# Performance work log

Hardware: AMD Instinct MI355X
Metric: run time of the kernel (lower is better)

## Reference

```python
import jax, jax.numpy as jnp
import numpy as np

N = 100000   # nodes
E = 1000000  # edges
DIN = 64
DH = 128     # num_hidden == out_dim
EPS = 1e-5


def setup_inputs() -> dict:
    key = jax.random.key(0)
    ks = jax.random.split(key, 16)
    x = jax.random.normal(ks[0], (N, DIN), jnp.float32)
    src = jax.random.randint(ks[1], (E,), 0, N)
    dst = jax.random.randint(ks[2], (E,), 0, N)
    dims = [(DIN, DH), (DH, DH), (DH, DH)]
    inp = {"x": x, "src": src, "dst": dst}
    for l, (di, do) in enumerate(dims):
        s = 1.0 / np.sqrt(di)
        inp[f"w_self{l}"] = jax.random.normal(ks[3 + 4 * l], (di, do), jnp.float32) * s
        inp[f"w_neigh{l}"] = jax.random.normal(ks[4 + 4 * l], (di, do), jnp.float32) * s
        inp[f"b{l}"] = jnp.zeros((do,), jnp.float32)
    # layernorm affine params for layers 0 and 1 (last layer has norm=None)
    for l in (0, 1):
        inp[f"g{l}"] = jnp.ones((DH,), jnp.float32)
        inp[f"be{l}"] = jnp.zeros((DH,), jnp.float32)
    return inp


def _layernorm(h, g, b):
    mu = jnp.mean(h, axis=-1, keepdims=True)
    var = jnp.mean(jnp.square(h - mu), axis=-1, keepdims=True)
    return (h - mu) * jax.lax.rsqrt(var + EPS) * g + b


def _sage_layer(h, src, dst, w_self, w_neigh, b, gamma, beta):
    # mean aggregation over incoming edges (DGL copy_u + mean)
    msg = h[src]                                            # [E, d_in]
    agg = jax.ops.segment_sum(msg, dst, num_segments=N)     # [N, d_in]
    deg = jax.ops.segment_sum(jnp.ones((E,), h.dtype), dst, num_segments=N)
    h_neigh = agg / jnp.where(deg > 0, deg, 1.0)[:, None]
    out = h @ w_self + h_neigh @ w_neigh + b
    out = jax.nn.relu(out)  # DGL applies activation before norm
    if gamma is not None:
        out = _layernorm(out, gamma, beta)
    return out


def reference(x, src, dst,
              w_self0, w_neigh0, b0,
              w_self1, w_neigh1, b1,
              w_self2, w_neigh2, b2,
              g0, be0, g1, be1):
    h = x  # dropout is identity in eval mode
    h = _sage_layer(h, src, dst, w_self0, w_neigh0, b0, g0, be0)
    h = _sage_layer(h, src, dst, w_self1, w_neigh1, b1, g1, be1)
    h = _sage_layer(h, src, dst, w_self2, w_neigh2, b2, None, None)
    return h
```

## Files before the change

kernel.cpp:

```cpp
#include <hip/hip_runtime.h>

#define NN   100000
#define NE   1000000
#define EPS  1e-5f
#define CAP  32
#define CPAD 16

typedef unsigned short ushort_t;
typedef unsigned int   uint_t;
typedef __attribute__((ext_vector_type(8))) __bf16 bf16x8;
typedef __attribute__((ext_vector_type(4))) float  f32x4;

static __device__ __forceinline__ ushort_t f2bf(float f) {
    uint_t u = __float_as_uint(f);
    u = u + 0x7fff + ((u >> 16) & 1);
    return (ushort_t)(u >> 16);
}
static __device__ __forceinline__ float bf2f(uint_t us) {
    return __uint_as_float(us << 16);
}

#define HALF_E 500000
#define EBH    1954
#define XBN    12500
#define WB0    64
#define WB1    128
#define PREP_BLOCKS (EBH + XBN + WB0 + WB1 + WB1)

static __device__ __forceinline__ void wprep_body(const float* __restrict__ wsf,
                                                  const float* __restrict__ wng,
                                                  __bf16* __restrict__ Bt, int DIN, int idx) {
    int K = 2 * DIN;
    if (idx >= 128 * K) return;
    int col = idx / K;
    int k   = idx % K;
    float v = (k < DIN) ? wsf[k * 128 + col] : wng[(k - DIN) * 128 + col];
    Bt[idx] = (__bf16)v;
}

__global__ __launch_bounds__(256) void k_prep(const int* __restrict__ src,
                                              const int* __restrict__ dst,
                                              int* __restrict__ cnt,
                                              int* __restrict__ slots,
                                              const float* __restrict__ x,
                                              ushort_t* __restrict__ xb,
                                              const float* __restrict__ ws0, const float* __restrict__ wn0, __bf16* __restrict__ Bt0,
                                              const float* __restrict__ ws1, const float* __restrict__ wn1, __bf16* __restrict__ Bt1,
                                              const float* __restrict__ ws2, const float* __restrict__ wn2, __bf16* __restrict__ Bt2) {
    int b = blockIdx.x;
    if (b < EBH) {
        int i = b * 256 + threadIdx.x;
        if (i < HALF_E) {
            int d0 = dst[i];
            int d1 = dst[i + HALF_E];
            int s0 = src[i];
            int s1 = src[i + HALF_E];
            int p0 = atomicAdd(&cnt[d0 * CPAD], 1);
            int p1 = atomicAdd(&cnt[d1 * CPAD], 1);
            if (p0 < CAP) __builtin_nontemporal_store(s0, &slots[d0 * CAP + p0]);
            if (p1 < CAP) __builtin_nontemporal_store(s1, &slots[d1 * CAP + p1]);
        }
        return;
    }
    b -= EBH;
    if (b < XBN) {
        int i = b * 256 + threadIdx.x;
        if (i < NN * 32) {
            float2 v = *(const float2*)(x + (size_t)i * 2);
            uint_t pk = (uint_t)f2bf(v.x) | ((uint_t)f2bf(v.y) << 16);
            *(uint_t*)(xb + (size_t)i * 2) = pk;
        }
        return;
    }
    b -= XBN;
    if (b < WB0) { wprep_body(ws0, wn0, Bt0, 64,  b * 256 + threadIdx.x); return; }
    b -= WB0;
    if (b < WB1) { wprep_body(ws1, wn1, Bt1, 128, b * 256 + threadIdx.x); return; }
    b -= WB1;
    wprep_body(ws2, wn2, Bt2, 128, b * 256 + threadIdx.x);
}

template <int DIN, bool DO_LN, bool OUT_F32>
__global__ __launch_bounds__(512, 4) void k_fused(const ushort_t* __restrict__ ha,
                                                  const int* __restrict__ slots,
                                                  const int* __restrict__ cnt,
                                                  const __bf16* __restrict__ Bt,
                                                  const float* __restrict__ bias,
                                                  const float* __restrict__ gamma,
                                                  const float* __restrict__ beta,
                                                  void* __restrict__ out) {
    constexpr int K     = 2 * DIN;
    constexpr int KS2   = DIN / 32;
    constexpr int EL    = (DIN == 64) ? 4 : 8;
    constexpr int PITCH = DIN + 8;
    int lane = threadIdx.x & 63;
    int w    = threadIdx.x >> 6;
    int n16  = lane & 15;
    int q    = lane >> 4;
    int base = blockIdx.x * 64;

    __shared__ float C[64 * 132];
    ushort_t* agg = (ushort_t*)C;

    int nb0  = w * 8;
    int degv = 0;
    if (lane < 8) {
        int nd = base + nb0 + lane;
        degv = (nd < NN) ? cnt[nd * CPAD] : 0;
    }
#pragma unroll
    for (int p = 0; p < 4; ++p) {
        int la = nb0 + 2 * p, lb = la + 1;
        int na = base + la,   nb = base + lb;
        int dega = __shfl(degv, 2 * p);
        int degb = __shfl(degv, 2 * p + 1);
        int ca = dega < CAP ? dega : CAP;
        int cb = degb < CAP ? degb : CAP;
        const int* sla = slots + (size_t)(na < NN ? na : NN - 1) * CAP;
        const int* slb = slots + (size_t)(nb < NN ? nb : NN - 1) * CAP;
        const int* slp = (lane < 32) ? sla : slb;
        int ivab = slp[lane & 31];

        float aa[EL], ab[EL];
#pragma unroll
        for (int k = 0; k < EL; ++k) { aa[k] = 0.f; ab[k] = 0.f; }

        int cam1 = ca > 0 ? ca - 1 : 0;
        int cbm1 = cb > 0 ? cb - 1 : 0;
        int cmax = ca > cb ? ca : cb;
        for (int t = 0; t < cmax; t += 8) {
#pragma unroll
            for (int hh = 0; hh < 2; ++hh) {
                int r  = t + hh * 4 + q;
                int ia = r < ca ? r : cam1;
                int ib = r < cb ? r : cbm1;
                int sa = __shfl(ivab, ia);
                int sb = __shfl(ivab, 32 + ib);
                if (r < ca) {
                    if (DIN == 64) {
                        uint2 v = *(const uint2*)(ha + (size_t)sa * 64 + n16 * 4);
                        aa[0] += bf2f(v.x & 0xffffu); aa[1] += bf2f(v.x >> 16);
                        aa[2] += bf2f(v.y & 0xffffu); aa[3] += bf2f(v.y >> 16);
                    } else {
                        uint4 v = *(const uint4*)(ha + (size_t)sa * 128 + n16 * 8);
                        aa[0] += bf2f(v.x & 0xffffu); aa[1] += bf2f(v.x >> 16);
                        aa[2] += bf2f(v.y & 0xffffu); aa[3] += bf2f(v.y >> 16);
                        aa[4] += bf2f(v.z & 0xffffu); aa[5] += bf2f(v.z >> 16);
                        aa[6] += bf2f(v.w & 0xffffu); aa[7] += bf2f(v.w >> 16);
                    }
                }
                if (r < cb) {
                    if (DIN == 64) {
                        uint2 v = *(const uint2*)(ha + (size_t)sb * 64 + n16 * 4);
                        ab[0] += bf2f(v.x & 0xffffu); ab[1] += bf2f(v.x >> 16);
                        ab[2] += bf2f(v.y & 0xffffu); ab[3] += bf2f(v.y >> 16);
                    } else {
                        uint4 v = *(const uint4*)(ha + (size_t)sb * 128 + n16 * 8);
                        ab[0] += bf2f(v.x & 0xffffu); ab[1] += bf2f(v.x >> 16);
                        ab[2] += bf2f(v.y & 0xffffu); ab[3] += bf2f(v.y >> 16);
                        ab[4] += bf2f(v.z & 0xffffu); ab[5] += bf2f(v.z >> 16);
                        ab[6] += bf2f(v.w & 0xffffu); ab[7] += bf2f(v.w >> 16);
                    }
                }
            }
        }
#pragma unroll
        for (int k = 0; k < EL; ++k) {
            aa[k] += __shfl_xor(aa[k], 16); aa[k] += __shfl_xor(aa[k], 32);
            ab[k] += __shfl_xor(ab[k], 16); ab[k] += __shfl_xor(ab[k], 32);
        }
        if (lane < 16) {
            float inva = 1.0f / (float)(dega > 0 ? dega : 1);
            float invb = 1.0f / (float)(degb > 0 ? degb : 1);
            if (DIN == 64) {
                uint2 oa, ob;
                oa.x = (uint_t)f2bf(aa[0] * inva) | ((uint_t)f2bf(aa[1] * inva) << 16);
                oa.y = (uint_t)f2bf(aa[2] * inva) | ((uint_t)f2bf(aa[3] * inva) << 16);
                ob.x = (uint_t)f2bf(ab[0] * invb) | ((uint_t)f2bf(ab[1] * invb) << 16);
                ob.y = (uint_t)f2bf(ab[2] * invb) | ((uint_t)f2bf(ab[3] * invb) << 16);
                *(uint2*)(agg + (size_t)la * PITCH + lane * 4) = oa;
                *(uint2*)(agg + (size_t)lb * PITCH + lane * 4) = ob;
            } else {
                uint4 oa, ob;
                oa.x = (uint_t)f2bf(aa[0] * inva) | ((uint_t)f2bf(aa[1] * inva) << 16);
                oa.y = (uint_t)f2bf(aa[2] * inva) | ((uint_t)f2bf(aa[3] * inva) << 16);
                oa.z = (uint_t)f2bf(aa[4] * inva) | ((uint_t)f2bf(aa[5] * inva) << 16);
                oa.w = (uint_t)f2bf(aa[6] * inva) | ((uint_t)f2bf(aa[7] * inva) << 16);
                ob.x = (uint_t)f2bf(ab[0] * invb) | ((uint_t)f2bf(ab[1] * invb) << 16);
                ob.y = (uint_t)f2bf(ab[2] * invb) | ((uint_t)f2bf(ab[3] * invb) << 16);
                ob.z = (uint_t)f2bf(ab[4] * invb) | ((uint_t)f2bf(ab[5] * invb) << 16);
                ob.w = (uint_t)f2bf(ab[6] * invb) | ((uint_t)f2bf(ab[7] * invb) << 16);
                *(uint4*)(agg + (size_t)la * PITCH + lane * 8) = oa;
                *(uint4*)(agg + (size_t)lb * PITCH + lane * 8) = ob;
            }
        }
    }
    __syncthreads();

    bf16x8 Bs[2][KS2];
#pragma unroll
    for (int hh = 0; hh < 2; ++hh)
#pragma unroll
        for (int ks = 0; ks < KS2; ++ks) {
            int col = w * 16 + n16;
            int k   = hh * DIN + ks * 32 + q * 8;
            Bs[hh][ks] = *(const bf16x8*)(Bt + (size_t)col * K + k);
        }

    int rowc[4];
#pragma unroll
    for (int ng = 0; ng < 4; ++ng) {
        int row  = base + ng * 16 + n16;
        rowc[ng] = row < NN ? row : NN - 1;
    }

    f32x4 acc[4] = {};

#pragma unroll
    for (int ks = 0; ks < KS2; ++ks) {
        bf16x8 a[4];
#pragma unroll
        for (int ng = 0; ng < 4; ++ng)
            a[ng] = *(const bf16x8*)(ha + (size_t)rowc[ng] * DIN + ks * 32 + q * 8);
#pragma unroll
        for (int ng = 0; ng < 4; ++ng)
            acc[ng] = __builtin_amdgcn_mfma_f32_16x16x32_bf16(a[ng], Bs[0][ks], acc[ng], 0, 0, 0);
    }
#pragma unroll
    for (int ks = 0; ks < KS2; ++ks) {
        bf16x8 a[4];
#pragma unroll
        for (int ng = 0; ng < 4; ++ng)
            a[ng] = *(const bf16x8*)(agg + (size_t)(ng * 16 + n16) * PITCH + ks * 32 + q * 8);
#pragma unroll
        for (int ng = 0; ng < 4; ++ng)
            acc[ng] = __builtin_amdgcn_mfma_f32_16x16x32_bf16(a[ng], Bs[1][ks], acc[ng], 0, 0, 0);
    }
    __syncthreads();

    {
        float bv = bias[w * 16 + n16];
#pragma unroll
        for (int ng = 0; ng < 4; ++ng)
#pragma unroll
            for (int r = 0; r < 4; ++r) {
                float v = acc[ng][r] + bv;
                C[(ng * 16 + q * 4 + r) * 132 + w * 16 + n16] = fmaxf(v, 0.f);
            }
    }
    __syncthreads();

    float g0v = 0.f, g1v = 0.f, b0v = 0.f, b1v = 0.f;
    if (DO_LN) {
        g0v = gamma[lane]; g1v = gamma[64 + lane];
        b0v = beta[lane];  b1v = beta[64 + lane];
    }
    for (int rr = 0; rr < 8; ++rr) {
        int lrow = w * 8 + rr;
        int node = base + lrow;
        if (node >= NN) break;
        float a0 = C[lrow * 132 + lane];
        float a1 = C[lrow * 132 + 64 + lane];
        float o0 = a0, o1 = a1;
        if (DO_LN) {
            float s = a0 + a1, qq = a0 * a0 + a1 * a1;
#pragma unroll
            for (int m = 1; m < 64; m <<= 1) {
                s  += __shfl_xor(s, m);
                qq += __shfl_xor(qq, m);
            }
            float mu  = s * (1.f / 128.f);
            float var = qq * (1.f / 128.f) - mu * mu;
            float rs  = rsqrtf(var + EPS);
            o0 = (a0 - mu) * rs * g0v + b0v;
            o1 = (a1 - mu) * rs * g1v + b1v;
        }
        if (OUT_F32) {
            ((float*)out)[(size_t)node * 128 + lane]      = o0;
            ((float*)out)[(size_t)node * 128 + 64 + lane] = o1;
        } else {
            ((ushort_t*)out)[(size_t)node * 128 + lane]      = f2bf(o0);
            ((ushort_t*)out)[(size_t)node * 128 + 64 + lane] = f2bf(o1);
        }
    }
}

extern "C" void kernel_launch(void* const* d_in, const int* in_sizes, int n_in,
                              void* d_out, int out_size, void* d_ws, size_t ws_size,
                              hipStream_t stream) {
    const float* x   = (const float*)d_in[0];
    const int*   src = (const int*)d_in[1];
    const int*   dst = (const int*)d_in[2];
    const float* ws0 = (const float*)d_in[3];
    const float* wn0 = (const float*)d_in[4];
    const float* b0  = (const float*)d_in[5];
    const float* ws1 = (const float*)d_in[6];
    const float* wn1 = (const float*)d_in[7];
    const float* b1  = (const float*)d_in[8];
    const float* ws2 = (const float*)d_in[9];
    const float* wn2 = (const float*)d_in[10];
    const float* b2  = (const float*)d_in[11];
    const float* g0  = (const float*)d_in[12];
    const float* be0 = (const float*)d_in[13];
    const float* g1  = (const float*)d_in[14];
    const float* be1 = (const float*)d_in[15];
    (void)in_sizes; (void)n_in; (void)out_size; (void)ws_size;

    char*  ws  = (char*)d_ws;
    size_t off = 0;
    auto alloc = [&](size_t bytes) -> void* {
        void* p = ws + off;
        off = (off + bytes + 255) & ~(size_t)255;
        return p;
    };
    ushort_t* xb     = (ushort_t*)alloc((size_t)NN * 64 * 2);
    ushort_t* h1b    = (ushort_t*)alloc((size_t)NN * 128 * 2);
    ushort_t* h2b    = (ushort_t*)alloc((size_t)NN * 128 * 2);
    int*      slots  = (int*)alloc((size_t)NN * CAP * 4);
    int*      cnt    = (int*)alloc((size_t)NN * CPAD * 4);
    __bf16*   Bt0    = (__bf16*)alloc(128 * 128 * 2);
    __bf16*   Bt1    = (__bf16*)alloc(128 * 256 * 2);
    __bf16*   Bt2    = (__bf16*)alloc(128 * 256 * 2);

    const int GB = (NN + 63) / 64;

    hipMemsetAsync(cnt, 0, (size_t)NN * CPAD * 4, stream);
    k_prep<<<PREP_BLOCKS, 256, 0, stream>>>(src, dst, cnt, slots, x, xb,
                                            ws0, wn0, Bt0, ws1, wn1, Bt1, ws2, wn2, Bt2);

    k_fused<64, true, false><<<GB, 512, 0, stream>>>(xb, slots, cnt, Bt0, b0, g0, be0, h1b);
    k_fused<128, true, false><<<GB, 512, 0, stream>>>(h1b, slots, cnt, Bt1, b1, g1, be1, h2b);
    k_fused<128, false, true><<<GB, 512, 0, stream>>>(h2b, slots, cnt, Bt2, b2, nullptr, nullptr, d_out);
}
```

Baseline: 435.8 us.

## Compact degree counters, interleave edge-scatter blocks with conversion blocks, guard slot loads

Removes the 16-int padding on the per-node degree counters, so the memset shrinks and counter reads in the fused kernel become dense. The prep grid is reordered so every eighth block does edge scatter while the other seven do x conversion and weight transposition, which spreads atomic traffic across the launch instead of front-loading it. Slot loads in the fused kernel are now skipped for lanes beyond the node's degree, avoiding reads of uninitialised slots. Dense counters risk more atomic contention on shared cache lines, and PREP_P must cover all edge and conversion blocks.

```diff
diff --git a/kernel.cpp b/kernel.cpp
--- a/kernel.cpp
+++ b/kernel.cpp
@@ -4,7 +4,6 @@
 #define NE   1000000
 #define EPS  1e-5f
 #define CAP  32
-#define CPAD 16
 
 typedef unsigned short ushort_t;
 typedef unsigned int   uint_t;
@@ -25,7 +24,7 @@
 #define XBN    12500
 #define WB0    64
 #define WB1    128
-#define PREP_BLOCKS (EBH + XBN + WB0 + WB1 + WB1)
+#define PREP_P 16384
 
 static __device__ __forceinline__ void wprep_body(const float* __restrict__ wsf,
                                                   const float* __restrict__ wng,
@@ -48,23 +47,25 @@
                                               const float* __restrict__ ws1, const float* __restrict__ wn1, __bf16* __restrict__ Bt1,
                                               const float* __restrict__ ws2, const float* __restrict__ wn2, __bf16* __restrict__ Bt2) {
     int b = blockIdx.x;
-    if (b < EBH) {
-        int i = b * 256 + threadIdx.x;
+    if ((b & 7) == 0) {
+        int fb = b >> 3;
+        if (fb >= EBH) return;
+        int i = fb * 256 + threadIdx.x;
         if (i < HALF_E) {
             int d0 = dst[i];
             int d1 = dst[i + HALF_E];
             int s0 = src[i];
             int s1 = src[i + HALF_E];
-            int p0 = atomicAdd(&cnt[d0 * CPAD], 1);
-            int p1 = atomicAdd(&cnt[d1 * CPAD], 1);
+            int p0 = atomicAdd(&cnt[d0], 1);
+            int p1 = atomicAdd(&cnt[d1], 1);
             if (p0 < CAP) __builtin_nontemporal_store(s0, &slots[d0 * CAP + p0]);
             if (p1 < CAP) __builtin_nontemporal_store(s1, &slots[d1 * CAP + p1]);
         }
         return;
     }
-    b -= EBH;
-    if (b < XBN) {
-        int i = b * 256 + threadIdx.x;
+    int ob = (b >> 3) * 7 + (b & 7) - 1;
+    if (ob < XBN) {
+        int i = ob * 256 + threadIdx.x;
         if (i < NN * 32) {
             float2 v = *(const float2*)(x + (size_t)i * 2);
             uint_t pk = (uint_t)f2bf(v.x) | ((uint_t)f2bf(v.y) << 16);
@@ -72,12 +73,12 @@
         }
         return;
     }
-    b -= XBN;
-    if (b < WB0) { wprep_body(ws0, wn0, Bt0, 64,  b * 256 + threadIdx.x); return; }
-    b -= WB0;
-    if (b < WB1) { wprep_body(ws1, wn1, Bt1, 128, b * 256 + threadIdx.x); return; }
-    b -= WB1;
-    wprep_body(ws2, wn2, Bt2, 128, b * 256 + threadIdx.x);
+    ob -= XBN;
+    if (ob < WB0) { wprep_body(ws0, wn0, Bt0, 64,  ob * 256 + threadIdx.x); return; }
+    ob -= WB0;
+    if (ob < WB1) { wprep_body(ws1, wn1, Bt1, 128, ob * 256 + threadIdx.x); return; }
+    ob -= WB1;
+    if (ob < WB1) { wprep_body(ws2, wn2, Bt2, 128, ob * 256 + threadIdx.x); }
 }
 
 template <int DIN, bool DO_LN, bool OUT_F32>
@@ -106,7 +107,7 @@
     int degv = 0;
     if (lane < 8) {
         int nd = base + nb0 + lane;
-        degv = (nd < NN) ? cnt[nd * CPAD] : 0;
+        degv = (nd < NN) ? cnt[nd] : 0;
     }
 #pragma unroll
     for (int p = 0; p < 4; ++p) {
@@ -119,7 +120,9 @@
         const int* sla = slots + (size_t)(na < NN ? na : NN - 1) * CAP;
         const int* slb = slots + (size_t)(nb < NN ? nb : NN - 1) * CAP;
         const int* slp = (lane < 32) ? sla : slb;
-        int ivab = slp[lane & 31];
+        int lim = (lane < 32) ? ca : cb;
+        int ivab = 0;
+        if ((lane & 31) < lim) ivab = slp[lane & 31];
 
         float aa[EL], ab[EL];
 #pragma unroll
@@ -317,16 +320,16 @@
     ushort_t* h1b    = (ushort_t*)alloc((size_t)NN * 128 * 2);
     ushort_t* h2b    = (ushort_t*)alloc((size_t)NN * 128 * 2);
     int*      slots  = (int*)alloc((size_t)NN * CAP * 4);
-    int*      cnt    = (int*)alloc((size_t)NN * CPAD * 4);
+    int*      cnt    = (int*)alloc((size_t)NN * 4);
     __bf16*   Bt0    = (__bf16*)alloc(128 * 128 * 2);
     __bf16*   Bt1    = (__bf16*)alloc(128 * 256 * 2);
     __bf16*   Bt2    = (__bf16*)alloc(128 * 256 * 2);
 
     const int GB = (NN + 63) / 64;
 
-    hipMemsetAsync(cnt, 0, (size_t)NN * CPAD * 4, stream);
-    k_prep<<<PREP_BLOCKS, 256, 0, stream>>>(src, dst, cnt, slots, x, xb,
-                                            ws0, wn0, Bt0, ws1, wn1, Bt1, ws2, wn2, Bt2);
+    hipMemsetAsync(cnt, 0, (size_t)NN * 4, stream);
+    k_prep<<<PREP_P, 256, 0, stream>>>(src, dst, cnt, slots, x, xb,
+                                       ws0, wn0, Bt0, ws1, wn1, Bt1, ws2, wn2, Bt2);
 
     k_fused<64, true, false><<<GB, 512, 0, stream>>>(xb, slots, cnt, Bt0, b0, g0, be0, h1b);
     k_fused<128, true, false><<<GB, 512, 0, stream>>>(h1b, slots, cnt, Bt1, b1, g1, be1, h2b);
```

New measurement: 462.1 us. 1.06x slower.

## Pre-bin edges by destination range before building adjacency slots

Applied to the files above, without the earlier changes.

Adds a binning kernel that partitions edges into 8 destination buckets of 12500 nodes, packing local dst and src into one word, using shared-memory counters and one global atomic per bucket per block. The slot-fill pass then reads each bucket in chunks, so the atomics on the count array and the scattered slot writes land in a localized node range that can stay cache-resident. The count array is no longer padded per node. This adds an extra kernel launch and an extra pass over the edges, and edges beyond a bucket's fixed capacity would be dropped.

```diff
diff --git a/kernel.cpp b/kernel.cpp
--- a/kernel.cpp
+++ b/kernel.cpp
@@ -4,7 +4,6 @@
 #define NE   1000000
 #define EPS  1e-5f
 #define CAP  32
-#define CPAD 16
 
 typedef unsigned short ushort_t;
 typedef unsigned int   uint_t;
@@ -22,10 +21,47 @@
 
 #define HALF_E 500000
 #define EBH    1954
+#define BCAP   131072
+#define BUCKN  12500
+
+__global__ __launch_bounds__(256) void k_bin(const int* __restrict__ src,
+                                             const int* __restrict__ dst,
+                                             int* __restrict__ cur,
+                                             uint_t* __restrict__ binned) {
+    __shared__ int bc[8];
+    __shared__ int bb[8];
+    int t = threadIdx.x;
+    if (t < 8) bc[t] = 0;
+    __syncthreads();
+    int i = blockIdx.x * 256 + t;
+    int g0 = 0, g1 = 0, l0 = 0, l1 = 0;
+    uint_t p0 = 0, p1 = 0;
+    bool ok = (i < HALF_E);
+    if (ok) {
+        int d0 = dst[i], d1 = dst[i + HALF_E];
+        int s0 = src[i], s1 = src[i + HALF_E];
+        g0 = d0 / BUCKN;  g1 = d1 / BUCKN;
+        p0 = ((uint_t)(d0 - g0 * BUCKN) << 17) | (uint_t)s0;
+        p1 = ((uint_t)(d1 - g1 * BUCKN) << 17) | (uint_t)s1;
+        l0 = atomicAdd(&bc[g0], 1);
+        l1 = atomicAdd(&bc[g1], 1);
+    }
+    __syncthreads();
+    if (t < 8) bb[t] = atomicAdd(&cur[t], bc[t]);
+    __syncthreads();
+    if (ok) {
+        int x0 = bb[g0] + l0;
+        int x1 = bb[g1] + l1;
+        if (x0 < BCAP) binned[(size_t)g0 * BCAP + x0] = p0;
+        if (x1 < BCAP) binned[(size_t)g1 * BCAP + x1] = p1;
+    }
+}
+
+#define FBL    2048
 #define XBN    12500
 #define WB0    64
 #define WB1    128
-#define PREP_BLOCKS (EBH + XBN + WB0 + WB1 + WB1)
+#define PREP_BLOCKS (FBL + XBN + WB0 + WB1 + WB1)
 
 static __device__ __forceinline__ void wprep_body(const float* __restrict__ wsf,
                                                   const float* __restrict__ wng,
@@ -38,8 +74,8 @@
     Bt[idx] = (__bf16)v;
 }
 
-__global__ __launch_bounds__(256) void k_prep(const int* __restrict__ src,
-                                              const int* __restrict__ dst,
+__global__ __launch_bounds__(256) void k_prep(const uint_t* __restrict__ binned,
+                                              const int* __restrict__ cur,
                                               int* __restrict__ cnt,
                                               int* __restrict__ slots,
                                               const float* __restrict__ x,
@@ -48,21 +84,25 @@
                                               const float* __restrict__ ws1, const float* __restrict__ wn1, __bf16* __restrict__ Bt1,
                                               const float* __restrict__ ws2, const float* __restrict__ wn2, __bf16* __restrict__ Bt2) {
     int b = blockIdx.x;
-    if (b < EBH) {
-        int i = b * 256 + threadIdx.x;
-        if (i < HALF_E) {
-            int d0 = dst[i];
-            int d1 = dst[i + HALF_E];
-            int s0 = src[i];
-            int s1 = src[i + HALF_E];
-            int p0 = atomicAdd(&cnt[d0 * CPAD], 1);
-            int p1 = atomicAdd(&cnt[d1 * CPAD], 1);
-            if (p0 < CAP) __builtin_nontemporal_store(s0, &slots[d0 * CAP + p0]);
-            if (p1 < CAP) __builtin_nontemporal_store(s1, &slots[d1 * CAP + p1]);
+    if (b < FBL) {
+        int g = b & 7;
+        int j = b >> 3;
+        int cg = cur[g]; if (cg > BCAP) cg = BCAP;
+        int chunk = (cg + 255) >> 8;
+        int beg = j * chunk;
+        int end = beg + chunk; if (end > cg) end = cg;
+        const uint_t* bp = binned + (size_t)g * BCAP;
+        int dbase = g * BUCKN;
+        for (int e = beg + threadIdx.x; e < end; e += 256) {
+            uint_t pk = bp[e];
+            int s = (int)(pk & 0x1FFFFu);
+            int d = dbase + (int)(pk >> 17);
+            int p = atomicAdd(&cnt[d], 1);
+            if (p < CAP) slots[d * CAP + p] = s;
         }
         return;
     }
-    b -= EBH;
+    b -= FBL;
     if (b < XBN) {
         int i = b * 256 + threadIdx.x;
         if (i < NN * 32) {
@@ -106,7 +146,7 @@
     int degv = 0;
     if (lane < 8) {
         int nd = base + nb0 + lane;
-        degv = (nd < NN) ? cnt[nd * CPAD] : 0;
+        degv = (nd < NN) ? cnt[nd] : 0;
     }
 #pragma unroll
     for (int p = 0; p < 4; ++p) {
@@ -317,15 +357,18 @@
     ushort_t* h1b    = (ushort_t*)alloc((size_t)NN * 128 * 2);
     ushort_t* h2b    = (ushort_t*)alloc((size_t)NN * 128 * 2);
     int*      slots  = (int*)alloc((size_t)NN * CAP * 4);
-    int*      cnt    = (int*)alloc((size_t)NN * CPAD * 4);
+    int*      cnt    = (int*)alloc((size_t)NN * 4 + 256);
+    int*      cur    = cnt + NN;
+    uint_t*   binned = (uint_t*)alloc((size_t)8 * BCAP * 4);
     __bf16*   Bt0    = (__bf16*)alloc(128 * 128 * 2);
     __bf16*   Bt1    = (__bf16*)alloc(128 * 256 * 2);
     __bf16*   Bt2    = (__bf16*)alloc(128 * 256 * 2);
 
     const int GB = (NN + 63) / 64;
 
-    hipMemsetAsync(cnt, 0, (size_t)NN * CPAD * 4, stream);
-    k_prep<<<PREP_BLOCKS, 256, 0, stream>>>(src, dst, cnt, slots, x, xb,
+    hipMemsetAsync(cnt, 0, (size_t)NN * 4 + 32, stream);
+    k_bin<<<EBH, 256, 0, stream>>>(src, dst, cur, binned);
+    k_prep<<<PREP_BLOCKS, 256, 0, stream>>>(binned, cur, cnt, slots, x, xb,
                                             ws0, wn0, Bt0, ws1, wn1, Bt1, ws2, wn2, Bt2);
 
     k_fused<64, true, false><<<GB, 512, 0, stream>>>(xb, slots, cnt, Bt0, b0, g0, be0, h1b);
```

Result: faster. 426.3 us (-2.2%).
